# Kernel tuning notes

Hardware: AMD Instinct MI355X
Metric: run time of the kernel (lower is better)

Reference implementation:

```python
import jax, jax.numpy as jnp
import numpy as np

B, S, H, L, V, T = 128, 512, 512, 2, 30, 64  # batch, enc len, hidden, layers, vocab, decode len


def _p(k, shape):
    return jax.random.normal(k, shape, jnp.float32) * 0.05


def setup_inputs() -> dict:
    key = jax.random.key(0)
    ks = jax.random.split(key, 24)
    inp = {"x": jax.random.normal(ks[0], (B, S, 2), jnp.float32)}
    inp["emb"] = _p(ks[1], (V, H))
    # encoder GRU (input dim 2 for layer 0, H for layer 1); PyTorch gate order r,z,n
    inp["enc_Wih0"] = _p(ks[2], (3 * H, 2));  inp["enc_Whh0"] = _p(ks[3], (3 * H, H))
    inp["enc_bih0"] = _p(ks[4], (3 * H,));    inp["enc_bhh0"] = _p(ks[5], (3 * H,))
    inp["enc_Wih1"] = _p(ks[6], (3 * H, H));  inp["enc_Whh1"] = _p(ks[7], (3 * H, H))
    inp["enc_bih1"] = _p(ks[8], (3 * H,));    inp["enc_bhh1"] = _p(ks[9], (3 * H,))
    # decoder GRU (input dim H)
    inp["dec_Wih0"] = _p(ks[10], (3 * H, H)); inp["dec_Whh0"] = _p(ks[11], (3 * H, H))
    inp["dec_bih0"] = _p(ks[12], (3 * H,));   inp["dec_bhh0"] = _p(ks[13], (3 * H,))
    inp["dec_Wih1"] = _p(ks[14], (3 * H, H)); inp["dec_Whh1"] = _p(ks[15], (3 * H, H))
    inp["dec_bih1"] = _p(ks[16], (3 * H,));   inp["dec_bhh1"] = _p(ks[17], (3 * H,))
    inp["fc_W"] = _p(ks[18], (V, 2 * H));     inp["fc_b"] = _p(ks[19], (V,))
    return inp


def gru_cell(xt, h, Wih, Whh, bih, bhh):
    gi = xt @ Wih.T + bih
    gh = h @ Whh.T + bhh
    i_r, i_z, i_n = jnp.split(gi, 3, axis=-1)
    h_r, h_z, h_n = jnp.split(gh, 3, axis=-1)
    r = jax.nn.sigmoid(i_r + h_r)
    z = jax.nn.sigmoid(i_z + h_z)
    n = jnp.tanh(i_n + r * h_n)
    return (1.0 - z) * n + z * h


def _forward(x, emb,
             enc_Wih0, enc_Whh0, enc_bih0, enc_bhh0,
             enc_Wih1, enc_Whh1, enc_bih1, enc_bhh1,
             dec_Wih0, dec_Whh0, dec_bih0, dec_bhh0,
             dec_Wih1, dec_Whh1, dec_bih1, dec_bhh1,
             fc_W, fc_b):
    b = x.shape[0]
    h0 = jnp.zeros((b, H), x.dtype)

    # ---- encoder: 2-layer GRU scanned over time ----
    def enc_step(hs, xt):
        a = gru_cell(xt, hs[0], enc_Wih0, enc_Whh0, enc_bih0, enc_bhh0)
        c = gru_cell(a, hs[1], enc_Wih1, enc_Whh1, enc_bih1, enc_bhh1)
        return (a, c), c

    (e0, e1), out_enc_t = jax.lax.scan(enc_step, (h0, h0), x.transpose(1, 0, 2))
    out_enc = out_enc_t.transpose(1, 0, 2)  # [B, S, H]

    def dec_step(carry, _):
        (d0, d1), tok = carry
        e = emb[tok]  # [B, H]
        n0 = gru_cell(e, d0, dec_Wih0, dec_Whh0, dec_bih0, dec_bhh0)
        n1 = gru_cell(n0, d1, dec_Wih1, dec_Whh1, dec_bih1, dec_bhh1)
        out_dec = n1  # [B, H]
        sim = jnp.einsum('bsh,bh->bs', out_enc, out_dec)  # [B, S]
        # faithful to nn.Softmax() implicit dim on 3-D [B,S,1] tensor -> dim=0 (batch)
        att_w = jax.nn.softmax(sim, axis=0)
        attention = jnp.einsum('bs,bsh->bh', att_w, out_enc)  # [B, H]
        logits = jnp.concatenate([out_dec, attention], axis=-1) @ fc_W.T + fc_b  # [B, V]
        tok_next = jnp.argmax(logits, axis=-1)
        return ((n0, n1), tok_next), logits

    tok0 = jnp.zeros((b,), jnp.int32)
    ((f0, f1), _), logits_t = jax.lax.scan(dec_step, ((e0, e1), tok0), None, length=T)
    vec_out = logits_t.transpose(1, 0, 2)  # [B, T, V]
    hidden = jnp.stack([f0, f1], axis=0)   # [n_layers, B, H]
    return vec_out, hidden


def reference(x, emb,
              enc_Wih0, enc_Whh0, enc_bih0, enc_bhh0,
              enc_Wih1, enc_Whh1, enc_bih1, enc_bhh1,
              dec_Wih0, dec_Whh0, dec_bih0, dec_bhh0,
              dec_Wih1, dec_Whh1, dec_bih1, dec_bhh1,
              fc_W, fc_b):
    return _forward(x, emb,
                    enc_Wih0, enc_Whh0, enc_bih0, enc_bhh0,
                    enc_Wih1, enc_Whh1, enc_bih1, enc_bhh1,
                    dec_Wih0, dec_Whh0, dec_bih0, dec_bhh0,
                    dec_Wih1, dec_Whh1, dec_bih1, dec_bhh1,
                    fc_W, fc_b)
```

## Files before the change

### kernel.cpp

```cpp
#include <hip/hip_runtime.h>
#include <math.h>

typedef short  s16x8 __attribute__((ext_vector_type(8)));
typedef float  f32x4 __attribute__((ext_vector_type(4)));
typedef unsigned short u16;

#define MFMA16(a, b, c) __builtin_amdgcn_mfma_f32_16x16x32_bf16((a), (b), (c), 0, 0, 0)

#define BB 128
#define SS 512
#define HH 512
#define VV 30
#define TT 64

__device__ __forceinline__ float b2f(u16 v) {
  union { unsigned int u; float f; } c; c.u = ((unsigned int)v) << 16; return c.f;
}
__device__ __forceinline__ u16 f2b(float f) {
  union { float f; unsigned int u; } c; c.f = f;
  unsigned int r = (c.u + 0x7FFFu + ((c.u >> 16) & 1u)) >> 16;
  return (u16)r;
}
__device__ __forceinline__ float sigm(float x) { return 1.f / (1.f + expf(-x)); }
__device__ __forceinline__ s16x8 ldf(const u16* p) { return *(const s16x8*)p; }


__device__ __forceinline__ void gru_dual(
    int bx,
    const u16* __restrict__ A1s, const int* __restrict__ gather,
    const u16* __restrict__ A2s,
    const u16* __restrict__ Wihs, const u16* __restrict__ Whhs,
    const float* __restrict__ bih, const float* __restrict__ bhh,
    float* __restrict__ hf, u16* __restrict__ hs_new,
    u16* __restrict__ oe, size_t oe_mstride)
{
  const int tid  = threadIdx.x;
  const int wave = tid >> 6, lane = tid & 63;
  const int lrow = lane & 15, lq = lane >> 4;
  const int j0 = (bx >> 1) * 16;
  const int m0 = (bx & 1) * 64 + wave * 16;

  const u16* a1p;
  if (gather) a1p = A1s + (size_t)gather[m0 + lrow] * 1024 + lq * 8;
  else        a1p = A1s + (size_t)(m0 + lrow) * 1024 + lq * 8;
  const u16* a2p = A2s + (size_t)(m0 + lrow) * 1024 + lq * 8;

  const u16* bp[6];
#pragma unroll
  for (int t = 0; t < 6; ++t) {
    int g = (t < 3) ? t : t - 3;
    const u16* W = (t < 3) ? Wihs : Whhs;
    bp[t] = W + (size_t)(g * HH + j0 + lrow) * 1024 + lq * 8;
  }

  f32x4 acc[6];
#pragma unroll
  for (int t = 0; t < 6; ++t) acc[t] = (f32x4){0.f, 0.f, 0.f, 0.f};

  for (int ks = 0; ks < HH; ks += 32) {
    s16x8 a1h = ldf(a1p), a1l = ldf(a1p + 512); a1p += 32;
    s16x8 a2h = ldf(a2p), a2l = ldf(a2p + 512); a2p += 32;
#pragma unroll
    for (int t = 0; t < 6; ++t) {
      s16x8 bh = ldf(bp[t]), bl = ldf(bp[t] + 512); bp[t] += 32;
      s16x8 ah = (t < 3) ? a1h : a2h;
      s16x8 al = (t < 3) ? a1l : a2l;
      acc[t] = MFMA16(ah, bh, acc[t]);
      acc[t] = MFMA16(ah, bl, acc[t]);
      acc[t] = MFMA16(al, bh, acc[t]);
    }
  }

  const int c = j0 + lrow;
  const float bir = bih[c], biz = bih[HH + c], bin = bih[2 * HH + c];
  const float bhr = bhh[c], bhz = bhh[HH + c], bhn = bhh[2 * HH + c];
#pragma unroll
  for (int r = 0; r < 4; ++r) {
    int m = m0 + lq * 4 + r;
    float ir = acc[0][r] + bir, iz = acc[1][r] + biz, inn = acc[2][r] + bin;
    float hr = acc[3][r] + bhr, hz = acc[4][r] + bhz, hn = acc[5][r] + bhn;
    float rr = sigm(ir + hr);
    float zz = sigm(iz + hz);
    float nn = tanhf(inn + rr * hn);
    float hp = hf[(size_t)m * HH + c];
    float hv = (1.f - zz) * nn + zz * hp;
    hf[(size_t)m * HH + c] = hv;
    u16 hi = f2b(hv);
    hs_new[(size_t)m * 1024 + c]       = hi;
    hs_new[(size_t)m * 1024 + 512 + c] = f2b(hv - b2f(hi));
    if (oe) oe[(size_t)m * oe_mstride + c] = hi;
  }
}

__device__ __forceinline__ void gru_l0(
    int bx, int p,
    const float* __restrict__ x, const float* __restrict__ Wih0,
    const u16* __restrict__ Whh0s,
    const float* __restrict__ bih0, const float* __restrict__ bhh0,
    const u16* __restrict__ As,
    float* __restrict__ af, u16* __restrict__ as_new)
{
  const int tid  = threadIdx.x;
  const int wave = tid >> 6, lane = tid & 63;
  const int lrow = lane & 15, lq = lane >> 4;
  const int j0 = bx * 16;
  const int mw = wave * 32;

  const u16* ap0 = As + (size_t)(mw + lrow) * 1024 + lq * 8;
  const u16* ap1 = As + (size_t)(mw + 16 + lrow) * 1024 + lq * 8;
  const u16* bp[3];
#pragma unroll
  for (int t = 0; t < 3; ++t)
    bp[t] = Whh0s + (size_t)(t * HH + j0 + lrow) * 1024 + lq * 8;

  f32x4 acc[2][3];
#pragma unroll
  for (int i = 0; i < 2; ++i)
#pragma unroll
    for (int t = 0; t < 3; ++t) acc[i][t] = (f32x4){0.f, 0.f, 0.f, 0.f};

  for (int ks = 0; ks < HH; ks += 32) {
    s16x8 a0h = ldf(ap0), a0l = ldf(ap0 + 512); ap0 += 32;
    s16x8 a1h = ldf(ap1), a1l = ldf(ap1 + 512); ap1 += 32;
#pragma unroll
    for (int t = 0; t < 3; ++t) {
      s16x8 bh = ldf(bp[t]), bl = ldf(bp[t] + 512); bp[t] += 32;
      acc[0][t] = MFMA16(a0h, bh, acc[0][t]);
      acc[0][t] = MFMA16(a0h, bl, acc[0][t]);
      acc[0][t] = MFMA16(a0l, bh, acc[0][t]);
      acc[1][t] = MFMA16(a1h, bh, acc[1][t]);
      acc[1][t] = MFMA16(a1h, bl, acc[1][t]);
      acc[1][t] = MFMA16(a1l, bh, acc[1][t]);
    }
  }

  const int c = j0 + lrow;
  const float bir = bih0[c], biz = bih0[HH + c], bin = bih0[2 * HH + c];
  const float bhr = bhh0[c], bhz = bhh0[HH + c], bhn = bhh0[2 * HH + c];
  const float wr0 = Wih0[(size_t)c * 2],            wr1 = Wih0[(size_t)c * 2 + 1];
  const float wz0 = Wih0[(size_t)(HH + c) * 2],     wz1 = Wih0[(size_t)(HH + c) * 2 + 1];
  const float wn0 = Wih0[(size_t)(2 * HH + c) * 2], wn1 = Wih0[(size_t)(2 * HH + c) * 2 + 1];
#pragma unroll
  for (int tm = 0; tm < 2; ++tm) {
#pragma unroll
    for (int r = 0; r < 4; ++r) {
      int m = mw + tm * 16 + lq * 4 + r;
      float x0 = x[((size_t)m * SS + p) * 2];
      float x1 = x[((size_t)m * SS + p) * 2 + 1];
      float ir  = bir + x0 * wr0 + x1 * wr1;
      float iz  = biz + x0 * wz0 + x1 * wz1;
      float inn = bin + x0 * wn0 + x1 * wn1;
      float hr = acc[tm][0][r] + bhr, hz = acc[tm][1][r] + bhz, hn = acc[tm][2][r] + bhn;
      float rr = sigm(ir + hr);
      float zz = sigm(iz + hz);
      float nn = tanhf(inn + rr * hn);
      float hp = af[(size_t)m * HH + c];
      float hv = (1.f - zz) * nn + zz * hp;
      af[(size_t)m * HH + c] = hv;
      u16 hi = f2b(hv);
      as_new[(size_t)m * 1024 + c]       = hi;
      as_new[(size_t)m * 1024 + 512 + c] = f2b(hv - b2f(hi));
    }
  }
}

__global__ __launch_bounds__(256) void enc_phase(
    int p,
    const float* __restrict__ x, const float* __restrict__ Wih0,
    const u16* __restrict__ Whh0s,
    const float* __restrict__ bih0, const float* __restrict__ bhh0,
    const u16* __restrict__ Wih1s, const u16* __restrict__ Whh1s,
    const float* __restrict__ bih1, const float* __restrict__ bhh1,
    const u16* abf_cur, u16* abf_new, float* af,
    const u16* cbf_cur, u16* cbf_new, float* cf,
    u16* out_enc)
{
  int bx = blockIdx.x;
  if (bx < 32) {
    if (p >= SS) return;
    gru_l0(bx, p, x, Wih0, Whh0s, bih0, bhh0, abf_cur, af, abf_new);
  } else {
    if (p == 0) return;
    u16* oe = out_enc + (size_t)(p - 1) * HH;
    gru_dual(bx - 32, abf_cur, nullptr, cbf_cur, Wih1s, Whh1s, bih1, bhh1,
             cf, cbf_new, oe, (size_t)SS * HH);
  }
}

__global__ __launch_bounds__(256) void dec_gru(
    const u16* A1s, const int* gather, const u16* A2s,
    const u16* __restrict__ Wihs, const u16* __restrict__ Whhs,
    const float* __restrict__ bih, const float* __restrict__ bhh,
    float* hf, u16* hs_new)
{
  gru_dual(blockIdx.x, A1s, gather, A2s, Wihs, Whhs, bih, bhh, hf, hs_new,
           nullptr, 0);
}

__global__ __launch_bounds__(256) void sim_kernel(
    const float* __restrict__ n1f, const u16* __restrict__ oe,
    float* __restrict__ simt)
{
  const int b = blockIdx.x >> 3, sc = blockIdx.x & 7;
  const int wave = threadIdx.x >> 6, lane = threadIdx.x & 63;
  float xr[8];
  const float* xp = n1f + (size_t)b * HH + lane * 8;
#pragma unroll
  for (int j = 0; j < 8; ++j) xr[j] = xp[j];
  int s0 = sc * 64 + wave * 16;
  for (int i = 0; i < 16; ++i) {
    int s = s0 + i;
    s16x8 ov = *(const s16x8*)(oe + ((size_t)b * SS + s) * HH + lane * 8);
    float acc = 0.f;
#pragma unroll
    for (int j = 0; j < 8; ++j) acc += xr[j] * b2f((u16)ov[j]);
    for (int off = 32; off; off >>= 1) acc += __shfl_down(acc, off);
    if (lane == 0) simt[(size_t)s * BB + b] = acc;
  }
}

__global__ __launch_bounds__(256) void attn_kernel(
    int tstep, const float* __restrict__ simt, const float* __restrict__ n1f,
    const u16* __restrict__ oe, const float* __restrict__ fcW,
    const float* __restrict__ fcb, float* __restrict__ dout,
    int* __restrict__ tok)
{
  __shared__ float wsm[SS];
  __shared__ float xv[2 * HH];
  __shared__ float lg[32];
  const int b = blockIdx.x, t = threadIdx.x;

  for (int s = t; s < SS; s += 256) {
    const float* row = simt + (size_t)s * BB;
    float mx = -1e30f;
    for (int i = 0; i < BB; ++i) mx = fmaxf(mx, row[i]);
    float e = 0.f;
    for (int i = 0; i < BB; ++i) e += expf(row[i] - mx);
    wsm[s] = expf(row[b] - mx) / e;
  }
  xv[t]       = n1f[(size_t)b * HH + t];
  xv[t + 256] = n1f[(size_t)b * HH + t + 256];
  __syncthreads();

  {
    float a0 = 0.f, a1 = 0.f;
    const u16* base = oe + (size_t)b * SS * HH;
    for (int s = 0; s < SS; ++s) {
      float w = wsm[s];
      a0 += w * b2f(base[(size_t)s * HH + t]);
      a1 += w * b2f(base[(size_t)s * HH + t + 256]);
    }
    xv[HH + t]       = a0;
    xv[HH + t + 256] = a1;
  }
  __syncthreads();

  int wave = t >> 6, lane = t & 63;
  for (int v = wave; v < VV; v += 4) {
    const float* wr = fcW + (size_t)v * (2 * HH);
    float acc = 0.f;
#pragma unroll
    for (int i = 0; i < 16; ++i) acc += xv[i * 64 + lane] * wr[i * 64 + lane];
    for (int off = 32; off; off >>= 1) acc += __shfl_down(acc, off);
    if (lane == 0) {
      float lv = acc + fcb[v];
      lg[v] = lv;
      dout[(size_t)b * (TT * VV) + (size_t)tstep * VV + v] = lv;
    }
  }
  __syncthreads();

  if (t == 0) {
    float best = lg[0]; int bi = 0;
    for (int v = 1; v < VV; ++v) if (lg[v] > best) { best = lg[v]; bi = v; }
    tok[b] = bi;
  }
}

__global__ __launch_bounds__(256) void splitk(
    const float* __restrict__ src, u16* __restrict__ dst, int n)
{
  int i = blockIdx.x * 256 + threadIdx.x;
  if (i >= n) return;
  int r = i >> 9, k = i & 511;
  float v = src[i];
  u16 hi = f2b(v);
  dst[(size_t)r * 1024 + k]       = hi;
  dst[(size_t)r * 1024 + 512 + k] = f2b(v - b2f(hi));
}

__global__ __launch_bounds__(256) void initk(
    float* af, float* cf, u16* b0, u16* b1, u16* b2, u16* b3, int* tok)
{
  int i = blockIdx.x * 256 + threadIdx.x;
  b0[i] = 0; b1[i] = 0; b2[i] = 0; b3[i] = 0;
  if (i < BB * HH) { af[i] = 0.f; cf[i] = 0.f; }
  if (i < BB) tok[i] = 0;
}

__global__ __launch_bounds__(256) void finalize(
    const float* __restrict__ d0, const float* __restrict__ d1,
    float* __restrict__ oh)
{
  int i = blockIdx.x * 256 + threadIdx.x;
  oh[i]           = d0[i];
  oh[BB * HH + i] = d1[i];
}

extern "C" void kernel_launch(void* const* d_in, const int* in_sizes, int n_in,
                              void* d_out, int out_size, void* d_ws, size_t ws_size,
                              hipStream_t stream) {
  const float* x     = (const float*)d_in[0];
  const float* emb   = (const float*)d_in[1];
  const float* eWih0 = (const float*)d_in[2];
  const float* eWhh0 = (const float*)d_in[3];
  const float* ebih0 = (const float*)d_in[4];
  const float* ebhh0 = (const float*)d_in[5];
  const float* eWih1 = (const float*)d_in[6];
  const float* eWhh1 = (const float*)d_in[7];
  const float* ebih1 = (const float*)d_in[8];
  const float* ebhh1 = (const float*)d_in[9];
  const float* dWih0 = (const float*)d_in[10];
  const float* dWhh0 = (const float*)d_in[11];
  const float* dbih0 = (const float*)d_in[12];
  const float* dbhh0 = (const float*)d_in[13];
  const float* dWih1 = (const float*)d_in[14];
  const float* dWhh1 = (const float*)d_in[15];
  const float* dbih1 = (const float*)d_in[16];
  const float* dbhh1 = (const float*)d_in[17];
  const float* fcW   = (const float*)d_in[18];
  const float* fcb   = (const float*)d_in[19];
  float* dout = (float*)d_out;

  char* wsb = (char*)d_ws;
  float* af   = (float*)(wsb + 0);
  float* cf   = (float*)(wsb + 262144);
  u16* ABF0   = (u16*)(wsb + 524288);
  u16* ABF1   = (u16*)(wsb + 786432);
  u16* CBF0   = (u16*)(wsb + 1048576);
  u16* CBF1   = (u16*)(wsb + 1310720);
  int* tok    = (int*)(wsb + 1572864);
  float* simt = (float*)(wsb + 1573376);
  u16* WeHH0  = (u16*)(wsb + 1835520);
  u16* WeIH1  = (u16*)(wsb + 4981248);
  u16* WeHH1  = (u16*)(wsb + 8126976);
  u16* WdIH0  = (u16*)(wsb + 11272704);
  u16* WdHH0  = (u16*)(wsb + 14418432);
  u16* WdIH1  = (u16*)(wsb + 17564160);
  u16* WdHH1  = (u16*)(wsb + 20709888);
  u16* EMBs   = (u16*)(wsb + 23855616);
  u16* oe     = (u16*)(wsb + 23917056);

  initk<<<512, 256, 0, stream>>>(af, cf, ABF0, ABF1, CBF0, CBF1, tok);

  const int WN = 3 * HH * HH;
  splitk<<<(WN + 255) / 256, 256, 0, stream>>>(eWhh0, WeHH0, WN);
  splitk<<<(WN + 255) / 256, 256, 0, stream>>>(eWih1, WeIH1, WN);
  splitk<<<(WN + 255) / 256, 256, 0, stream>>>(eWhh1, WeHH1, WN);
  splitk<<<(WN + 255) / 256, 256, 0, stream>>>(dWih0, WdIH0, WN);
  splitk<<<(WN + 255) / 256, 256, 0, stream>>>(dWhh0, WdHH0, WN);
  splitk<<<(WN + 255) / 256, 256, 0, stream>>>(dWih1, WdIH1, WN);
  splitk<<<(WN + 255) / 256, 256, 0, stream>>>(dWhh1, WdHH1, WN);
  splitk<<<(VV * HH + 255) / 256, 256, 0, stream>>>(emb, EMBs, VV * HH);

  const u16* pa = ABF0; u16* pa_n = ABF1;
  const u16* pc = CBF0; u16* pc_n = CBF1;
  for (int p = 0; p <= SS; ++p) {
    enc_phase<<<96, 256, 0, stream>>>(p, x, eWih0, WeHH0, ebih0, ebhh0,
                                      WeIH1, WeHH1, ebih1, ebhh1,
                                      pa, pa_n, af, pc, pc_n, cf, oe);
    const u16* tp;
    tp = pa; pa = pa_n; pa_n = (u16*)tp;
    tp = pc; pc = pc_n; pc_n = (u16*)tp;
  }
  const u16* d0c = ABF0; u16* d0n = ABF1;
  const u16* d1c = CBF1; u16* d1n = CBF0;

  for (int t = 0; t < TT; ++t) {
    dec_gru<<<64, 256, 0, stream>>>(EMBs, tok, d0c, WdIH0, WdHH0,
                                    dbih0, dbhh0, af, d0n);
    const u16* tp = d0c; d0c = d0n; d0n = (u16*)tp;
    dec_gru<<<64, 256, 0, stream>>>(d0c, nullptr, d1c, WdIH1, WdHH1,
                                    dbih1, dbhh1, cf, d1n);
    tp = d1c; d1c = d1n; d1n = (u16*)tp;
    sim_kernel<<<1024, 256, 0, stream>>>(cf, oe, simt);
    attn_kernel<<<128, 256, 0, stream>>>(t, simt, cf, oe, fcW, fcb, dout, tok);
  }

  finalize<<<256, 256, 0, stream>>>(af, cf, dout + (size_t)BB * TT * VV);
}
```

Baseline: 27.43 ms.

## Replace per-step kernel launches with persistent kernels using grid barriers

Runs the encoder and the decoder each as one persistent kernel. A software grid-wide barrier (atomic counter plus generation flag) replaces the 513 encoder launches and the 4×64 decoder launches. This removes launch overhead and launch gaps on the serial recurrence. In exchange it depends on all blocks being co-resident, which holds for 96/128 blocks, and it places the barrier counters in the hidden-state region of the output buffer, which is overwritten at the end.

```diff
diff --git a/kernel.cpp b/kernel.cpp
--- a/kernel.cpp
+++ b/kernel.cpp
@@ -23,6 +23,24 @@
 }
 __device__ __forceinline__ float sigm(float x) { return 1.f / (1.f + expf(-x)); }
 __device__ __forceinline__ s16x8 ldf(const u16* p) { return *(const s16x8*)p; }
+
+__device__ __forceinline__ void gbar(int* cnt, int* gen, int nb) {
+  __syncthreads();
+  if (threadIdx.x == 0) {
+    __threadfence();
+    int g = __hip_atomic_load(gen, __ATOMIC_RELAXED, __HIP_MEMORY_SCOPE_AGENT);
+    int a = __hip_atomic_fetch_add(cnt, 1, __ATOMIC_ACQ_REL, __HIP_MEMORY_SCOPE_AGENT);
+    if (a == nb - 1) {
+      __hip_atomic_store(cnt, 0, __ATOMIC_RELAXED, __HIP_MEMORY_SCOPE_AGENT);
+      __hip_atomic_fetch_add(gen, 1, __ATOMIC_ACQ_REL, __HIP_MEMORY_SCOPE_AGENT);
+    } else {
+      while (__hip_atomic_load(gen, __ATOMIC_ACQUIRE, __HIP_MEMORY_SCOPE_AGENT) == g)
+        __builtin_amdgcn_s_sleep(8);
+    }
+    __threadfence();
+  }
+  __syncthreads();
+}
 
 
 __device__ __forceinline__ void gru_dual(
@@ -164,44 +182,37 @@
   }
 }
 
-__global__ __launch_bounds__(256) void enc_phase(
-    int p,
+__global__ __launch_bounds__(256) void enc_persist(
     const float* __restrict__ x, const float* __restrict__ Wih0,
     const u16* __restrict__ Whh0s,
     const float* __restrict__ bih0, const float* __restrict__ bhh0,
     const u16* __restrict__ Wih1s, const u16* __restrict__ Whh1s,
     const float* __restrict__ bih1, const float* __restrict__ bhh1,
-    const u16* abf_cur, u16* abf_new, float* af,
-    const u16* cbf_cur, u16* cbf_new, float* cf,
-    u16* out_enc)
-{
-  int bx = blockIdx.x;
-  if (bx < 32) {
-    if (p >= SS) return;
-    gru_l0(bx, p, x, Wih0, Whh0s, bih0, bhh0, abf_cur, af, abf_new);
-  } else {
-    if (p == 0) return;
-    u16* oe = out_enc + (size_t)(p - 1) * HH;
-    gru_dual(bx - 32, abf_cur, nullptr, cbf_cur, Wih1s, Whh1s, bih1, bhh1,
-             cf, cbf_new, oe, (size_t)SS * HH);
-  }
-}
-
-__global__ __launch_bounds__(256) void dec_gru(
-    const u16* A1s, const int* gather, const u16* A2s,
-    const u16* __restrict__ Wihs, const u16* __restrict__ Whhs,
-    const float* __restrict__ bih, const float* __restrict__ bhh,
-    float* hf, u16* hs_new)
-{
-  gru_dual(blockIdx.x, A1s, gather, A2s, Wihs, Whhs, bih, bhh, hf, hs_new,
-           nullptr, 0);
-}
-
-__global__ __launch_bounds__(256) void sim_kernel(
-    const float* __restrict__ n1f, const u16* __restrict__ oe,
+    u16* A0, u16* A1, float* af, u16* C0, u16* C1, float* cf,
+    u16* out_enc, int* bcnt, int* bgen)
+{
+  const int bx = blockIdx.x;
+  u16 *pa = A0, *pan = A1, *pc = C0, *pcn = C1;
+  for (int p = 0; p <= SS; ++p) {
+    if (bx < 32) {
+      if (p < SS) gru_l0(bx, p, x, Wih0, Whh0s, bih0, bhh0, pa, af, pan);
+    } else {
+      if (p > 0)
+        gru_dual(bx - 32, pa, nullptr, pc, Wih1s, Whh1s, bih1, bhh1,
+                 cf, pcn, out_enc + (size_t)(p - 1) * HH, (size_t)SS * HH);
+    }
+    if (p < SS) gbar(bcnt, bgen, 96);
+    u16* tp;
+    tp = pa; pa = pan; pan = tp;
+    tp = pc; pc = pcn; pcn = tp;
+  }
+}
+
+__device__ __forceinline__ void sim_body(
+    int vb, const float* __restrict__ n1f, const u16* __restrict__ oe,
     float* __restrict__ simt)
 {
-  const int b = blockIdx.x >> 3, sc = blockIdx.x & 7;
+  const int b = vb >> 3, sc = vb & 7;
   const int wave = threadIdx.x >> 6, lane = threadIdx.x & 63;
   float xr[8];
   const float* xp = n1f + (size_t)b * HH + lane * 8;
@@ -219,8 +230,9 @@
   }
 }
 
-__global__ __launch_bounds__(256) void attn_kernel(
-    int tstep, const float* __restrict__ simt, const float* __restrict__ n1f,
+__device__ __forceinline__ void attn_body(
+    int b, int tstep,
+    const float* __restrict__ simt, const float* __restrict__ n1f,
     const u16* __restrict__ oe, const float* __restrict__ fcW,
     const float* __restrict__ fcb, float* __restrict__ dout,
     int* __restrict__ tok)
@@ -228,7 +240,7 @@
   __shared__ float wsm[SS];
   __shared__ float xv[2 * HH];
   __shared__ float lg[32];
-  const int b = blockIdx.x, t = threadIdx.x;
+  const int t = threadIdx.x;
 
   for (int s = t; s < SS; s += 256) {
     const float* row = simt + (size_t)s * BB;
@@ -275,6 +287,49 @@
     for (int v = 1; v < VV; ++v) if (lg[v] > best) { best = lg[v]; bi = v; }
     tok[b] = bi;
   }
+  __syncthreads();
+}
+
+__global__ __launch_bounds__(256) void dec_persist(
+    const u16* __restrict__ EMBs,
+    u16* D0c, u16* D0n, u16* D1c, u16* D1n,
+    const u16* __restrict__ WdIH0, const u16* __restrict__ WdHH0,
+    const float* __restrict__ dbih0, const float* __restrict__ dbhh0,
+    const u16* __restrict__ WdIH1, const u16* __restrict__ WdHH1,
+    const float* __restrict__ dbih1, const float* __restrict__ dbhh1,
+    float* af, float* cf, const u16* __restrict__ oe,
+    const float* __restrict__ fcW, const float* __restrict__ fcb,
+    float* simt, float* dout, int* tok, int* bcnt, int* bgen)
+{
+  const int bx = blockIdx.x;
+  u16 *d0c = D0c, *d0n = D0n, *d1c = D1c, *d1n = D1n;
+
+  for (int ts = 0; ts < TT; ++ts) {
+    if (bx < 64)
+      gru_dual(bx, EMBs, tok, d0c, WdIH0, WdHH0, dbih0, dbhh0, af, d0n,
+               nullptr, 0);
+    gbar(bcnt, bgen, 128);
+    u16* tp = d0c; d0c = d0n; d0n = tp;
+
+    if (bx < 64)
+      gru_dual(bx, d0c, nullptr, d1c, WdIH1, WdHH1, dbih1, dbhh1, cf, d1n,
+               nullptr, 0);
+    gbar(bcnt, bgen, 128);
+    tp = d1c; d1c = d1n; d1n = tp;
+
+    for (int vb = bx; vb < 1024; vb += 128)
+      sim_body(vb, cf, oe, simt);
+    gbar(bcnt, bgen, 128);
+
+    attn_body(bx, ts, simt, cf, oe, fcW, fcb, dout, tok);
+    if (ts < TT - 1) gbar(bcnt, bgen, 128);
+  }
+
+  float* oh = dout + (size_t)BB * TT * VV;
+  for (int i = bx * 256 + threadIdx.x; i < BB * HH; i += 128 * 256) {
+    oh[i]           = af[i];
+    oh[BB * HH + i] = cf[i];
+  }
 }
 
 __global__ __launch_bounds__(256) void splitk(
@@ -290,21 +345,14 @@
 }
 
 __global__ __launch_bounds__(256) void initk(
-    float* af, float* cf, u16* b0, u16* b1, u16* b2, u16* b3, int* tok)
+    float* af, float* cf, u16* b0, u16* b1, u16* b2, u16* b3, int* tok,
+    int* bars)
 {
   int i = blockIdx.x * 256 + threadIdx.x;
   b0[i] = 0; b1[i] = 0; b2[i] = 0; b3[i] = 0;
   if (i < BB * HH) { af[i] = 0.f; cf[i] = 0.f; }
   if (i < BB) tok[i] = 0;
-}
-
-__global__ __launch_bounds__(256) void finalize(
-    const float* __restrict__ d0, const float* __restrict__ d1,
-    float* __restrict__ oh)
-{
-  int i = blockIdx.x * 256 + threadIdx.x;
-  oh[i]           = d0[i];
-  oh[BB * HH + i] = d1[i];
+  if (i < 2) bars[i] = 0;
 }
 
 extern "C" void kernel_launch(void* const* d_in, const int* in_sizes, int n_in,
@@ -351,7 +399,9 @@
   u16* EMBs   = (u16*)(wsb + 23855616);
   u16* oe     = (u16*)(wsb + 23917056);
 
-  initk<<<512, 256, 0, stream>>>(af, cf, ABF0, ABF1, CBF0, CBF1, tok);
+  int* bars = (int*)(dout + (size_t)BB * TT * VV);
+
+  initk<<<512, 256, 0, stream>>>(af, cf, ABF0, ABF1, CBF0, CBF1, tok, bars);
 
   const int WN = 3 * HH * HH;
   splitk<<<(WN + 255) / 256, 256, 0, stream>>>(eWhh0, WeHH0, WN);
@@ -363,29 +413,14 @@
   splitk<<<(WN + 255) / 256, 256, 0, stream>>>(dWhh1, WdHH1, WN);
   splitk<<<(VV * HH + 255) / 256, 256, 0, stream>>>(emb, EMBs, VV * HH);
 
-  const u16* pa = ABF0; u16* pa_n = ABF1;
-  const u16* pc = CBF0; u16* pc_n = CBF1;
-  for (int p = 0; p <= SS; ++p) {
-    enc_phase<<<96, 256, 0, stream>>>(p, x, eWih0, WeHH0, ebih0, ebhh0,
+  enc_persist<<<96, 256, 0, stream>>>(x, eWih0, WeHH0, ebih0, ebhh0,
                                       WeIH1, WeHH1, ebih1, ebhh1,
-                                      pa, pa_n, af, pc, pc_n, cf, oe);
-    const u16* tp;
-    tp = pa; pa = pa_n; pa_n = (u16*)tp;
-    tp = pc; pc = pc_n; pc_n = (u16*)tp;
-  }
-  const u16* d0c = ABF0; u16* d0n = ABF1;
-  const u16* d1c = CBF1; u16* d1n = CBF0;
-
-  for (int t = 0; t < TT; ++t) {
-    dec_gru<<<64, 256, 0, stream>>>(EMBs, tok, d0c, WdIH0, WdHH0,
-                                    dbih0, dbhh0, af, d0n);
-    const u16* tp = d0c; d0c = d0n; d0n = (u16*)tp;
-    dec_gru<<<64, 256, 0, stream>>>(d0c, nullptr, d1c, WdIH1, WdHH1,
-                                    dbih1, dbhh1, cf, d1n);
-    tp = d1c; d1c = d1n; d1n = (u16*)tp;
-    sim_kernel<<<1024, 256, 0, stream>>>(cf, oe, simt);
-    attn_kernel<<<128, 256, 0, stream>>>(t, simt, cf, oe, fcW, fcb, dout, tok);
-  }
-
-  finalize<<<256, 256, 0, stream>>>(af, cf, dout + (size_t)BB * TT * VV);
-}
+                                      ABF0, ABF1, af, CBF0, CBF1, cf,
+                                      oe, bars, bars + 1);
+
+  dec_persist<<<128, 256, 0, stream>>>(EMBs, ABF0, ABF1, CBF1, CBF0,
+                                       WdIH0, WdHH0, dbih0, dbhh0,
+                                       WdIH1, WdHH1, dbih1, dbhh1,
+                                       af, cf, oe, fcW, fcb,
+                                       simt, dout, tok, bars, bars + 1);
+}
```

New measurement: 42.92 ms. 56.4% more time.
